# Optimization experiments

Measured on AMD Instinct MI355X. Metric: run time of the kernel, lower is better.

The kernel has to match this reference:

```python
import jax, jax.numpy as jnp
import numpy as np

WEIGHTS = (1.428, 40.097)


def setup_inputs() -> dict:
    key = jax.random.key(0)
    k1, k2 = jax.random.split(key)
    N, C, H, W = 32, 2, 512, 512
    inputs = jax.random.uniform(k1, (N, C, H, W), dtype=jnp.float32)
    targets = jax.random.randint(k2, (N, H, W), 0, C, dtype=jnp.int32)
    return {"inputs": inputs, "targets": targets}


def reference(inputs, targets):
    # Lovasz hinge-style loss, vectorized over all N*C rows at once.
    N, C, H, W = inputs.shape
    P = H * W
    x = inputs.reshape(N, C, P)                                   # [N,C,P]
    # masks[n,c,p] = (targets[n,p] == c)
    masks = (targets.reshape(N, 1, P) == jnp.arange(C, dtype=targets.dtype).reshape(1, C, 1)).astype(x.dtype)

    distance = jnp.abs(masks - x)                                 # [N,C,P]
    order = jnp.argsort(-distance, axis=-1)                       # descending sort indices
    d_sorted = jnp.take_along_axis(distance, order, axis=-1)
    m_sorted = jnp.take_along_axis(masks, order, axis=-1)

    msum = jnp.sum(m_sorted, axis=-1, keepdims=True)              # [N,C,1]
    inter = msum - jnp.cumsum(m_sorted, axis=-1)
    union = msum + jnp.cumsum(1.0 - m_sorted, axis=-1)
    iou = 1.0 - inter / union                                     # [N,C,P]
    # gradient of Lovasz extension: first-difference of iou
    grad = jnp.concatenate([iou[..., :1], iou[..., 1:] - iou[..., :-1]], axis=-1)

    per_row = jnp.sum(d_sorted * grad, axis=-1)                   # [N,C]

    # rows skipped when mask empty AND no prediction > 0.25
    empty = (jnp.sum(masks, axis=-1) == 0) & (jnp.sum(x > 0.25, axis=-1) == 0)
    valid = jnp.logical_not(empty)                                # [N,C]

    w = jnp.asarray(WEIGHTS, dtype=x.dtype)                       # [C]
    total = jnp.sum(per_row * w[None, :] * valid.astype(x.dtype))
    non_empty = jnp.sum(valid.astype(x.dtype))
    return total / N / non_empty
```

## Files before the change

### kernel.cpp

```cpp
#include <hip/hip_runtime.h>

#define NN   32
#define CCH  2
#define PP   (512*512)
#define RR   (NN*CCH)
#define NB   2048
#define BPR  16
#define CHUNK (PP/BPR)
#define HT   512
#define ST   256

static_assert(CHUNK % (HT*4) == 0, "");
static_assert(NB % ST == 0, "");
static_assert(CHUNK < 65536, "packed 16-bit cnt would overflow");

__device__ __forceinline__ double iou_f(double msum, unsigned k, unsigned cs) {
    if (k == 0u) return 0.0;
    if (msum == 0.0) return 1.0;
    const double dk = (double)k, dcs = (double)cs;
    return 1.0 - (msum - dcs) / (msum + dk - dcs);
}

__global__ __launch_bounds__(HT) void hist_kernel(
        const float* __restrict__ x, const int* __restrict__ tgt,
        unsigned* __restrict__ g_hist, unsigned* __restrict__ g_pos)
{
    __shared__ unsigned s_hist[NB];
    __shared__ unsigned s_pos[HT/64];

    const int r = blockIdx.x / BPR, b = blockIdx.x % BPR;
    const int n = r / CCH, c = r % CCH;
    const int tid = threadIdx.x;

    for (int i = tid; i < NB; i += HT) s_hist[i] = 0u;
    __syncthreads();

    const float* xrow = x   + (size_t)r * PP;
    const int*   trow = tgt + (size_t)n * PP;
    const int start = b * CHUNK;

    unsigned pos = 0;
    #pragma unroll
    for (int it = 0; it < CHUNK/(HT*4); ++it) {
        const int p = start + it*(HT*4) + tid*4;
        const float4 xv = *reinterpret_cast<const float4*>(xrow + p);
        const int4   tv = *reinterpret_cast<const int4*>(trow + p);
        #pragma unroll
        for (int j = 0; j < 4; ++j) {
            const float xs = (j==0) ? xv.x : (j==1) ? xv.y : (j==2) ? xv.z : xv.w;
            const int   ts = (j==0) ? tv.x : (j==1) ? tv.y : (j==2) ? tv.z : tv.w;
            const unsigned m = (ts == c) ? 1u : 0u;
            const float d  = m ? (1.0f - xs) : xs;
            int bk = (int)(d * (float)NB);
            bk = bk > NB-1 ? NB-1 : bk;
            atomicAdd(&s_hist[bk], 0x10000u | m);
            pos += (xs > 0.25f) ? 1u : 0u;
        }
    }

    for (int off = 32; off; off >>= 1) pos += __shfl_down(pos, off);
    if ((tid & 63) == 0) s_pos[tid >> 6] = pos;
    __syncthreads();
    if (tid == 0) {
        unsigned t = 0;
        #pragma unroll
        for (int w = 0; w < HT/64; ++w) t += s_pos[w];
        g_pos[blockIdx.x] = t;
    }

    const size_t base = (size_t)blockIdx.x * NB;
    for (int i = tid; i < NB; i += HT) g_hist[base+i] = s_hist[i];
}

__global__ __launch_bounds__(ST) void scan_kernel(
        const unsigned* __restrict__ g_hist, const unsigned* __restrict__ g_pos,
        float* __restrict__ g_row, float* __restrict__ g_valid)
{
    __shared__ unsigned m_cnt[NB];
    __shared__ unsigned m_ones[NB];
    __shared__ unsigned long long s_scan[ST];
    __shared__ double   s_red[ST/64];

    const int r = blockIdx.x;
    const int tid = threadIdx.x;

    for (int i = tid; i < NB; i += ST) {
        unsigned cs = 0, os = 0;
        #pragma unroll
        for (int b = 0; b < BPR; ++b) {
            const unsigned v = g_hist[((size_t)(r*BPR + b))*NB + i];
            cs += v >> 16; os += v & 0xffffu;
        }
        m_cnt[i] = cs; m_ones[i] = os;
    }
    __syncthreads();

    constexpr int Q = NB/ST;
    unsigned lc = 0, lo = 0;
    #pragma unroll
    for (int q = 0; q < Q; ++q) {
        const int bk = NB-1 - (tid*Q + q);
        lc += m_cnt[bk]; lo += m_ones[bk];
    }

    const unsigned long long v = ((unsigned long long)lc << 32) | (unsigned long long)lo;
    s_scan[tid] = v;
    __syncthreads();
    for (int off = 1; off < ST; off <<= 1) {
        const unsigned long long add = (tid >= off) ? s_scan[tid-off] : 0ULL;
        __syncthreads();
        s_scan[tid] += add;
        __syncthreads();
    }
    const unsigned long long excl = s_scan[tid] - v;
    const unsigned long long tot  = s_scan[ST-1];
    const unsigned msum = (unsigned)(tot & 0xffffffffULL);

    unsigned k  = (unsigned)(excl >> 32);
    unsigned cs = (unsigned)(excl & 0xffffffffULL);
    const double dmsum = (double)msum;

    double acc = 0.0;
    #pragma unroll
    for (int q = 0; q < Q; ++q) {
        const int bk = NB-1 - (tid*Q + q);
        const unsigned c_ = m_cnt[bk];
        if (c_) {
            const double ip = iou_f(dmsum, k, cs);
            k += c_; cs += m_ones[bk];
            const double in_ = iou_f(dmsum, k, cs);
            const double dmid = ((double)bk + 0.5) * (1.0 / (double)NB);
            acc += dmid * (in_ - ip);
        }
    }

    for (int off = 32; off; off >>= 1) acc += __shfl_down(acc, off);
    if ((tid & 63) == 0) s_red[tid >> 6] = acc;
    __syncthreads();
    if (tid == 0) {
        double t = 0.0;
        #pragma unroll
        for (int w = 0; w < ST/64; ++w) t += s_red[w];
        unsigned pos = 0;
        for (int b = 0; b < BPR; ++b) pos += g_pos[r*BPR + b];
        const bool valid = !(msum == 0u && pos == 0u);
        const double W[CCH] = {1.428, 40.097};
        g_row[r]   = valid ? (float)(t * W[r % CCH]) : 0.f;
        g_valid[r] = valid ? 1.f : 0.f;
    }
}

__global__ __launch_bounds__(64) void final_kernel(
        const float* __restrict__ g_row, const float* __restrict__ g_valid,
        float* __restrict__ out)
{
    const int tid = threadIdx.x;
    double t = (double)g_row[tid];
    double v = (double)g_valid[tid];
    for (int off = 32; off; off >>= 1) { t += __shfl_down(t, off); v += __shfl_down(v, off); }
    if (tid == 0) out[0] = (float)(t / (double)NN / v);
}

extern "C" void kernel_launch(void* const* d_in, const int* in_sizes, int n_in,
                              void* d_out, int out_size, void* d_ws, size_t ws_size,
                              hipStream_t stream) {
    const float* x   = (const float*)d_in[0];
    const int*   tgt = (const int*)d_in[1];
    float* out = (float*)d_out;

    const size_t SZH = (size_t)RR * BPR * NB;
    unsigned* g_hist = (unsigned*)d_ws;
    unsigned* g_pos  = g_hist + SZH;
    float*    g_row  = (float*)(g_pos + RR*BPR);
    float*    g_valid = g_row + RR;

    hist_kernel<<<RR*BPR, HT, 0, stream>>>(x, tgt, g_hist, g_pos);
    scan_kernel<<<RR, ST, 0, stream>>>(g_hist, g_pos, g_row, g_valid);
    final_kernel<<<1, 64, 0, stream>>>(g_row, g_valid, out);
}
```

Before: 32.36 us.

## Halve histogram bins, widen per-thread loads, fold final reduce into scan via ticket

Three changes. The bin count drops from 2048 to 1024, which shrinks shared-memory init, global histogram traffic and scan work, at the cost of coarser distance quantization and more atomic contention per bin. Each thread now loads 8 elements per iteration instead of 4. The separate final-reduction kernel is removed: the last scan block to finish, detected with an atomic ticket counter, performs the final sum, which saves one kernel launch.

```diff
diff --git a/kernel.cpp b/kernel.cpp
--- a/kernel.cpp
+++ b/kernel.cpp
@@ -4,15 +4,16 @@
 #define CCH  2
 #define PP   (512*512)
 #define RR   (NN*CCH)
-#define NB   2048
+#define NB   1024
 #define BPR  16
 #define CHUNK (PP/BPR)
 #define HT   512
 #define ST   256
 
-static_assert(CHUNK % (HT*4) == 0, "");
+static_assert(CHUNK % (HT*8) == 0, "");
 static_assert(NB % ST == 0, "");
 static_assert(CHUNK < 65536, "packed 16-bit cnt would overflow");
+static_assert(RR <= 64, "final reduce assumes one wave");
 
 __device__ __forceinline__ double iou_f(double msum, unsigned k, unsigned cs) {
     if (k == 0u) return 0.0;
@@ -23,7 +24,8 @@
 
 __global__ __launch_bounds__(HT) void hist_kernel(
         const float* __restrict__ x, const int* __restrict__ tgt,
-        unsigned* __restrict__ g_hist, unsigned* __restrict__ g_pos)
+        unsigned* __restrict__ g_hist, unsigned* __restrict__ g_pos,
+        unsigned* __restrict__ g_ticket)
 {
     __shared__ unsigned s_hist[NB];
     __shared__ unsigned s_pos[HT/64];
@@ -31,6 +33,8 @@
     const int r = blockIdx.x / BPR, b = blockIdx.x % BPR;
     const int n = r / CCH, c = r % CCH;
     const int tid = threadIdx.x;
+
+    if (blockIdx.x == 0 && tid == 0) *g_ticket = 0u;
 
     for (int i = tid; i < NB; i += HT) s_hist[i] = 0u;
     __syncthreads();
@@ -41,20 +45,22 @@
 
     unsigned pos = 0;
     #pragma unroll
-    for (int it = 0; it < CHUNK/(HT*4); ++it) {
-        const int p = start + it*(HT*4) + tid*4;
-        const float4 xv = *reinterpret_cast<const float4*>(xrow + p);
-        const int4   tv = *reinterpret_cast<const int4*>(trow + p);
+    for (int it = 0; it < CHUNK/(HT*8); ++it) {
+        const int p = start + it*(HT*8) + tid*8;
+        const float4 xv0 = *reinterpret_cast<const float4*>(xrow + p);
+        const float4 xv1 = *reinterpret_cast<const float4*>(xrow + p + 4);
+        const int4   tv0 = *reinterpret_cast<const int4*>(trow + p);
+        const int4   tv1 = *reinterpret_cast<const int4*>(trow + p + 4);
+        const float xs[8] = {xv0.x,xv0.y,xv0.z,xv0.w, xv1.x,xv1.y,xv1.z,xv1.w};
+        const int   ts[8] = {tv0.x,tv0.y,tv0.z,tv0.w, tv1.x,tv1.y,tv1.z,tv1.w};
         #pragma unroll
-        for (int j = 0; j < 4; ++j) {
-            const float xs = (j==0) ? xv.x : (j==1) ? xv.y : (j==2) ? xv.z : xv.w;
-            const int   ts = (j==0) ? tv.x : (j==1) ? tv.y : (j==2) ? tv.z : tv.w;
-            const unsigned m = (ts == c) ? 1u : 0u;
-            const float d  = m ? (1.0f - xs) : xs;
+        for (int j = 0; j < 8; ++j) {
+            const unsigned m = (ts[j] == c) ? 1u : 0u;
+            const float d  = m ? (1.0f - xs[j]) : xs[j];
             int bk = (int)(d * (float)NB);
             bk = bk > NB-1 ? NB-1 : bk;
             atomicAdd(&s_hist[bk], 0x10000u | m);
-            pos += (xs > 0.25f) ? 1u : 0u;
+            pos += (xs[j] > 0.25f) ? 1u : 0u;
         }
     }
 
@@ -74,12 +80,14 @@
 
 __global__ __launch_bounds__(ST) void scan_kernel(
         const unsigned* __restrict__ g_hist, const unsigned* __restrict__ g_pos,
-        float* __restrict__ g_row, float* __restrict__ g_valid)
+        float* __restrict__ g_row, float* __restrict__ g_valid,
+        unsigned* __restrict__ g_ticket, float* __restrict__ out)
 {
     __shared__ unsigned m_cnt[NB];
     __shared__ unsigned m_ones[NB];
     __shared__ unsigned long long s_scan[ST];
     __shared__ double   s_red[ST/64];
+    __shared__ unsigned s_ticket;
 
     const int r = blockIdx.x;
     const int tid = threadIdx.x;
@@ -147,18 +155,25 @@
         const double W[CCH] = {1.428, 40.097};
         g_row[r]   = valid ? (float)(t * W[r % CCH]) : 0.f;
         g_valid[r] = valid ? 1.f : 0.f;
+        __threadfence();
+        s_ticket = atomicAdd(g_ticket, 1u);
     }
-}
+    __syncthreads();
 
-__global__ __launch_bounds__(64) void final_kernel(
-        const float* __restrict__ g_row, const float* __restrict__ g_valid,
-        float* __restrict__ out)
-{
-    const int tid = threadIdx.x;
-    double t = (double)g_row[tid];
-    double v = (double)g_valid[tid];
-    for (int off = 32; off; off >>= 1) { t += __shfl_down(t, off); v += __shfl_down(v, off); }
-    if (tid == 0) out[0] = (float)(t / (double)NN / v);
+    if (s_ticket == RR - 1) {
+        __threadfence();
+        if (tid < 64) {
+            const volatile float* vr = g_row;
+            const volatile float* vv = g_valid;
+            double t = (tid < RR) ? (double)vr[tid] : 0.0;
+            double vl = (tid < RR) ? (double)vv[tid] : 0.0;
+            for (int off = 32; off; off >>= 1) {
+                t  += __shfl_down(t, off);
+                vl += __shfl_down(vl, off);
+            }
+            if (tid == 0) out[0] = (float)(t / (double)NN / vl);
+        }
+    }
 }
 
 extern "C" void kernel_launch(void* const* d_in, const int* in_sizes, int n_in,
@@ -169,12 +184,12 @@
     float* out = (float*)d_out;
 
     const size_t SZH = (size_t)RR * BPR * NB;
-    unsigned* g_hist = (unsigned*)d_ws;
-    unsigned* g_pos  = g_hist + SZH;
-    float*    g_row  = (float*)(g_pos + RR*BPR);
+    unsigned* g_hist  = (unsigned*)d_ws;
+    unsigned* g_pos   = g_hist + SZH;
+    float*    g_row   = (float*)(g_pos + RR*BPR);
     float*    g_valid = g_row + RR;
+    unsigned* g_ticket = (unsigned*)(g_valid + RR);
 
-    hist_kernel<<<RR*BPR, HT, 0, stream>>>(x, tgt, g_hist, g_pos);
-    scan_kernel<<<RR, ST, 0, stream>>>(g_hist, g_pos, g_row, g_valid);
-    final_kernel<<<1, 64, 0, stream>>>(g_row, g_valid, out);
+    hist_kernel<<<RR*BPR, HT, 0, stream>>>(x, tgt, g_hist, g_pos, g_ticket);
+    scan_kernel<<<RR, ST, 0, stream>>>(g_hist, g_pos, g_row, g_valid, g_ticket, out);
 }
```

After: 30.51 us. 5.7% less time.
